# Kernel tuning notes

Measured on AMD Instinct MI355X. Metric: run time of the kernel, lower is better.

The kernel has to match this reference:

```python
import jax, jax.numpy as jnp
import numpy as np

B, T, D, H = 2, 2048, 1024, 16
HD = D // H  # head_dim = 64

def setup_inputs() -> dict:
    key = jax.random.key(0)
    ks = jax.random.split(key, 5)
    s = 0.02
    return {
        "x": jax.random.normal(ks[0], (B, T, D), dtype=jnp.float32),
        "w_qkv": jax.random.normal(ks[1], (3 * D, D), dtype=jnp.float32) * s,
        "b_qkv": jax.random.normal(ks[2], (3 * D,), dtype=jnp.float32) * s,
        "w_proj": jax.random.normal(ks[3], (D, D), dtype=jnp.float32) * s,
        "b_proj": jax.random.normal(ks[4], (D,), dtype=jnp.float32) * s,
    }

def reference(x, w_qkv, b_qkv, w_proj, b_proj):
    b, t, c = x.shape
    h, hd = H, HD
    scale = hd ** -0.5
    # qkv projection (torch Linear: x @ W^T + b)
    qkv = x @ w_qkv.T + b_qkv                      # [b, t, 3c]
    q, k, v = jnp.split(qkv, 3, axis=-1)
    # b t (h d) -> b h t d
    reshape = lambda z: z.reshape(b, t, h, hd).transpose(0, 2, 1, 3)
    q, k, v = reshape(q), reshape(k), reshape(v)
    scores = jnp.einsum("bhqd,bhkd->bhqk", q, k) * scale  # [b, h, t, t]
    causal = jnp.triu(jnp.ones((t, t), dtype=bool), k=1)   # True above diag
    scores = jnp.where(causal[None, None], -jnp.inf, scores)
    attn = jax.nn.softmax(scores, axis=-1)
    out = jnp.einsum("bhqk,bhkd->bhqd", attn, v)            # [b, h, t, d]
    out = out.transpose(0, 2, 1, 3).reshape(b, t, c)        # b h t d -> b t (h d)
    return out @ w_proj.T + b_proj
```

## Files before the change

kernel.cpp:

```cpp
#include <hip/hip_runtime.h>
#include <hip/hip_bf16.h>

#define Bq 2
#define Tq 2048
#define Dq 1024
#define Hq 16
#define HDq 64

typedef __attribute__((ext_vector_type(8))) short short8;
typedef __attribute__((ext_vector_type(4))) float f32x4;

__device__ __forceinline__ unsigned short f2bf(float f) {
  union { float f; unsigned int i; } v; v.f = f;
  unsigned int r = v.i + 0x7fffu + ((v.i >> 16) & 1u);
  return (unsigned short)(r >> 16);
}

__device__ __forceinline__ short8 cvt8(const float* __restrict__ g) {
  const float4* gp = (const float4*)g;
  float4 x0 = gp[0], x1 = gp[1];
  short8 v;
  v[0] = (short)f2bf(x0.x); v[1] = (short)f2bf(x0.y);
  v[2] = (short)f2bf(x0.z); v[3] = (short)f2bf(x0.w);
  v[4] = (short)f2bf(x1.x); v[5] = (short)f2bf(x1.y);
  v[6] = (short)f2bf(x1.z); v[7] = (short)f2bf(x1.w);
  return v;
}

__device__ __forceinline__ void async_cp16(const void* g, void* l) {
  __builtin_amdgcn_global_load_lds(
      (const __attribute__((address_space(1))) void*)g,
      (__attribute__((address_space(3))) void*)l, 16, 0, 0);
}

__device__ __forceinline__ void permswap(unsigned &a, unsigned &b) {
  asm("v_permlane32_swap_b32 %0, %1" : "+v"(a), "+v"(b));
  asm("v_permlane16_swap_b32 %0, %1" : "+v"(a), "+v"(b));
}

constexpr int NXC = (Bq * Tq * Dq) / 8;
constexpr int NW1C = (3 * Dq * Dq) / 8;
constexpr int NW2C = (Dq * Dq) / 8;

#define QSCL 0.18033688011112042f

__global__ __launch_bounds__(256)
void cvt_all(const float* __restrict__ x, const float* __restrict__ w1,
             const float* __restrict__ w2, unsigned short* __restrict__ xo,
             unsigned short* __restrict__ w1o, unsigned short* __restrict__ w2o)
{
  int i = blockIdx.x * 256 + threadIdx.x;
  const float* src; unsigned short* dst; int j;
  if (i < NXC)              { src = x;  dst = xo;  j = i; }
  else if (i < NXC + NW1C)  { src = w1; dst = w1o; j = i - NXC; }
  else                      { src = w2; dst = w2o; j = i - NXC - NW1C; }
  *(short8*)&dst[(size_t)j * 8] = cvt8(src + (size_t)j * 8);
}


__global__ __launch_bounds__(512, 2)
void gemm_qkv_8p(const unsigned short* __restrict__ Ab,
                 const unsigned short* __restrict__ Wb,
                 const float* __restrict__ bias, int K,
                 unsigned short* __restrict__ qo, unsigned short* __restrict__ ko,
                 unsigned short* __restrict__ vo)
{
  __shared__ unsigned short As[2][256 * 64];
  __shared__ unsigned short Bs[2][256 * 64];

  const int t = threadIdx.x;
  const int lane = t & 63, w = t >> 6;
  const int fr = lane & 15, qd = lane >> 4;
  const int wmi = w >> 2, wni = w & 3;
  const int m0 = blockIdx.y * 256, n0 = blockIdx.x * 256;
  const int arow_base = wmi * 128;
  const int brow_base = wni * 64;

  const int Gr0 = t >> 3;
  const int Gr1 = 64 + Gr0;
  const int Gc  = (t & 7) ^ (Gr0 & 7);

#define STAGE_HALF(kt1, hh, bufi) do {                                         \
    const unsigned short* _sb = ((hh) < 2) ? Ab + (size_t)m0 * K               \
                                           : Wb + (size_t)n0 * K;              \
    unsigned short* _lb = ((hh) < 2) ? &As[bufi][0] : &Bs[bufi][0];            \
    const int _h = (hh) & 1;                                                   \
    async_cp16(_sb + (size_t)(_h * 128 + Gr0) * K + (kt1) * 64 + Gc * 8,       \
               _lb + _h * 8192 + t * 8);                                       \
    async_cp16(_sb + (size_t)(_h * 128 + Gr1) * K + (kt1) * 64 + Gc * 8,       \
               _lb + _h * 8192 + 4096 + t * 8);                                \
  } while (0)

#define READ_AF(rg) do {                                                       \
    _Pragma("unroll")                                                          \
    for (int ibs = 0; ibs < 4; ibs++) {                                        \
      const int r = arow_base + (rg) * 64 + ibs * 16 + fr;                     \
      af[ibs][0] = *(const short8*)&As[c][r * 64 + ((qd ^ (r & 7)) * 8)];      \
      af[ibs][1] = *(const short8*)&As[c][r * 64 + (((4 + qd) ^ (r & 7)) * 8)];\
    } } while (0)

#define READ_BF(cg) do {                                                       \
    _Pragma("unroll")                                                          \
    for (int jbs = 0; jbs < 2; jbs++) {                                        \
      const int r = brow_base + (cg) * 32 + jbs * 16 + fr;                     \
      bf[jbs][0] = *(const short8*)&Bs[c][r * 64 + ((qd ^ (r & 7)) * 8)];      \
      bf[jbs][1] = *(const short8*)&Bs[c][r * 64 + (((4 + qd) ^ (r & 7)) * 8)];\
    } } while (0)

#define MM16(rg, cg) do {                                                      \
    __builtin_amdgcn_s_setprio(1);                                             \
    _Pragma("unroll")                                                          \
    for (int ibs = 0; ibs < 4; ibs++)                                          \
      _Pragma("unroll")                                                        \
      for (int jbs = 0; jbs < 2; jbs++) {                                      \
        acc[(rg)*4+ibs][(cg)*2+jbs] = __builtin_amdgcn_mfma_f32_16x16x32_bf16( \
            af[ibs][0], bf[jbs][0], acc[(rg)*4+ibs][(cg)*2+jbs], 0, 0, 0);     \
        acc[(rg)*4+ibs][(cg)*2+jbs] = __builtin_amdgcn_mfma_f32_16x16x32_bf16( \
            af[ibs][1], bf[jbs][1], acc[(rg)*4+ibs][(cg)*2+jbs], 0, 0, 0);     \
      }                                                                        \
    __builtin_amdgcn_s_setprio(0); } while (0)

#define BAR() do { asm volatile("" ::: "memory");                              \
    __builtin_amdgcn_s_barrier(); asm volatile("" ::: "memory"); } while (0)

  f32x4 acc[8][4] = {};
  short8 af[4][2], bf[2][2];

  STAGE_HALF(0, 0, 0); STAGE_HALF(0, 1, 0);
  STAGE_HALF(0, 2, 0); STAGE_HALF(0, 3, 0);

  const int KT = K >> 6;
  for (int kt = 0; kt < KT; kt++) {
    const int c = kt & 1;
    const bool pf = (kt + 1 < KT);
    if (pf) {
      STAGE_HALF(kt + 1, 0, c ^ 1);
      asm volatile("s_waitcnt vmcnt(2)" ::: "memory");
    } else {
      asm volatile("s_waitcnt vmcnt(0)" ::: "memory");
    }
    __builtin_amdgcn_s_barrier();
    READ_AF(0); READ_BF(0);
    BAR();
    MM16(0, 0);
    BAR();
    READ_BF(1);
    if (pf) STAGE_HALF(kt + 1, 1, c ^ 1);
    BAR();
    MM16(0, 1);
    BAR();
    READ_AF(1);
    if (pf) STAGE_HALF(kt + 1, 2, c ^ 1);
    BAR();
    MM16(1, 1);
    BAR();
    READ_BF(0);
    if (pf) STAGE_HALF(kt + 1, 3, c ^ 1);
    BAR();
    MM16(1, 0);
    BAR();
  }

  #pragma unroll
  for (int jb = 0; jb < 4; jb++) {
    int col = n0 + wni * 64 + jb * 16 + fr;
    float bv = bias[col];
    int which = col >> 10;
    int rem = col & 1023;
    int hh = rem >> 6, dd = rem & 63;
    #pragma unroll
    for (int ib = 0; ib < 8; ib++) {
      int row4 = m0 + wmi * 128 + ib * 16 + qd * 4;
      int bb = row4 >> 11, tt = row4 & (Tq - 1);
      if (which == 2) {
        unsigned lo = (unsigned)f2bf(acc[ib][jb][0] + bv)
                    | ((unsigned)f2bf(acc[ib][jb][1] + bv) << 16);
        unsigned hi = (unsigned)f2bf(acc[ib][jb][2] + bv)
                    | ((unsigned)f2bf(acc[ib][jb][3] + bv) << 16);
        uint2 pk; pk.x = lo; pk.y = hi;
        *(uint2*)&vo[((size_t)(bb * Hq + hh) * HDq + dd) * Tq + tt] = pk;
      } else {
        unsigned short* dst = (which == 0) ? qo : ko;
        float scl = (which == 0) ? QSCL : 1.0f;
        #pragma unroll
        for (int r = 0; r < 4; r++)
          dst[((size_t)(bb * Hq + hh) * Tq + tt + r) * HDq + dd] =
              f2bf((acc[ib][jb][r] + bv) * scl);
      }
    }
  }
#undef STAGE_HALF
#undef READ_AF
#undef READ_BF
#undef MM16
#undef BAR
}

template<int EPI, int BM_, int BN_>
__global__ __launch_bounds__(256)
void gemm_bt(const unsigned short* __restrict__ Ab, const unsigned short* __restrict__ Wb,
             const float* __restrict__ bias, float* __restrict__ outp,
             int K, int N,
             unsigned short* __restrict__ qo, unsigned short* __restrict__ ko,
             unsigned short* __restrict__ vo)
{
  constexpr int WM = BM_ / 2, WN = BN_ / 2;
  constexpr int NI = WM / 16;
  constexpr int NJ = WN / 16;
  constexpr int NAI = BM_ / 32;
  constexpr int NBI = BN_ / 32;
  __shared__ unsigned short As[2 * BM_ * 32];
  __shared__ unsigned short Bs[2 * BN_ * 32];

  const int t = threadIdx.x;
  const int lane = t & 63, w = t >> 6;
  const int m0 = blockIdx.y * BM_, n0 = blockIdx.x * BN_;
  const int fr = lane & 15, qd = lane >> 4;
  const int wm = (w >> 1) * WM, wn = (w & 1) * WN;

  f32x4 acc[NI][NJ] = {};

  for (int k0 = 0; k0 < K; k0 += 64) {
    __syncthreads();
    #pragma unroll
    for (int j = 0; j < NAI; j++) {
      int G = j * 256 + t;
      int panel = G / (BM_ * 4), rowg = (G / 4) % BM_, colg = G & 3;
      async_cp16(Ab + (size_t)(m0 + rowg) * K + k0 + panel * 32 + colg * 8, &As[G * 8]);
    }
    #pragma unroll
    for (int j = 0; j < NBI; j++) {
      int G = j * 256 + t;
      int panel = G / (BN_ * 4), rowg = (G / 4) % BN_, colg = G & 3;
      async_cp16(Wb + (size_t)(n0 + rowg) * K + k0 + panel * 32 + colg * 8, &Bs[G * 8]);
    }
    __syncthreads();
    #pragma unroll
    for (int kh = 0; kh < 2; kh++) {
      short8 af[NI], bf[NJ];
      #pragma unroll
      for (int ib = 0; ib < NI; ib++)
        af[ib] = *(const short8*)&As[kh * (BM_ * 32) + (wm + ib * 16 + fr) * 32 + qd * 8];
      #pragma unroll
      for (int jb = 0; jb < NJ; jb++)
        bf[jb] = *(const short8*)&Bs[kh * (BN_ * 32) + (wn + jb * 16 + fr) * 32 + qd * 8];
      #pragma unroll
      for (int ib = 0; ib < NI; ib++)
        #pragma unroll
        for (int jb = 0; jb < NJ; jb++)
          acc[ib][jb] = __builtin_amdgcn_mfma_f32_16x16x32_bf16(af[ib], bf[jb], acc[ib][jb], 0, 0, 0);
    }
  }

  #pragma unroll
  for (int jb = 0; jb < NJ; jb++) {
    int col = n0 + wn + jb * 16 + fr;
    float bv = bias[col];
    if (EPI == 0) {
      int which = col >> 10;
      int rem = col & 1023;
      int hh = rem >> 6, dd = rem & 63;
      #pragma unroll
      for (int ib = 0; ib < NI; ib++) {
        int row4 = m0 + wm + ib * 16 + qd * 4;
        int bb = row4 >> 11, tt = row4 & (Tq - 1);
        if (which == 2) {
          unsigned lo = (unsigned)f2bf(acc[ib][jb][0] + bv)
                      | ((unsigned)f2bf(acc[ib][jb][1] + bv) << 16);
          unsigned hi = (unsigned)f2bf(acc[ib][jb][2] + bv)
                      | ((unsigned)f2bf(acc[ib][jb][3] + bv) << 16);
          uint2 pk; pk.x = lo; pk.y = hi;
          *(uint2*)&vo[((size_t)(bb * Hq + hh) * HDq + dd) * Tq + tt] = pk;
        } else {
          unsigned short* dst = (which == 0) ? qo : ko;
          float scl = (which == 0) ? QSCL : 1.0f;
          #pragma unroll
          for (int r = 0; r < 4; r++)
            dst[((size_t)(bb * Hq + hh) * Tq + tt + r) * HDq + dd] =
                f2bf((acc[ib][jb][r] + bv) * scl);
        }
      }
    } else {
      #pragma unroll
      for (int ib = 0; ib < NI; ib++)
        #pragma unroll
        for (int r = 0; r < 4; r++) {
          int row = m0 + wm + ib * 16 + qd * 4 + r;
          outp[(size_t)row * N + col] = acc[ib][jb][r] + bv;
        }
    }
  }
}


template<bool DIAG>
__device__ __forceinline__ void strip_iter(
    const unsigned short* __restrict__ Ksb, const unsigned short* __restrict__ Vtsb,
    const short8 (&aq)[2], const short8 ones,
    int fr, int qd, int off0, int off1, int thr,
    f32x4 (&oacc)[4], f32x4& lacc)
{
  short8 bk[4][2];
  #pragma unroll
  for (int nb = 0; nb < 4; nb++) {
    bk[nb][0] = *(const short8*)&Ksb[(nb * 16 + fr) * 64 + off0];
    bk[nb][1] = *(const short8*)&Ksb[(nb * 16 + fr) * 64 + off1];
  }
  f32x4 s4[4] = {};
  __builtin_amdgcn_s_setprio(1);
  #pragma unroll
  for (int nb = 0; nb < 4; nb++)
    s4[nb] = __builtin_amdgcn_mfma_f32_16x16x32_bf16(bk[nb][0], aq[0], s4[nb], 0, 0, 0);
  #pragma unroll
  for (int nb = 0; nb < 4; nb++)
    s4[nb] = __builtin_amdgcn_mfma_f32_16x16x32_bf16(bk[nb][1], aq[1], s4[nb], 0, 0, 0);
  __builtin_amdgcn_s_setprio(0);

  unsigned x[4][2];
  #pragma unroll
  for (int nb = 0; nb < 4; nb++) {
    float p[4];
    #pragma unroll
    for (int reg = 0; reg < 4; reg++) {
      p[reg] = exp2f(s4[nb][reg]);
      if (DIAG && (nb * 16 + qd * 4 + reg) > thr) p[reg] = 0.f;
    }
    asm("v_cvt_pk_bf16_f32 %0, %1, %2" : "=v"(x[nb][0]) : "v"(p[0]), "v"(p[1]));
    asm("v_cvt_pk_bf16_f32 %0, %1, %2" : "=v"(x[nb][1]) : "v"(p[2]), "v"(p[3]));
  }
  permswap(x[0][0], x[1][0]);
  permswap(x[0][1], x[1][1]);
  permswap(x[2][0], x[3][0]);
  permswap(x[2][1], x[3][1]);

  short8 ap0, ap1;
  {
    union { unsigned u[4]; short8 s; } c0, c1;
    c0.u[0] = x[0][0]; c0.u[1] = x[0][1]; c0.u[2] = x[1][0]; c0.u[3] = x[1][1];
    c1.u[0] = x[2][0]; c1.u[1] = x[2][1]; c1.u[2] = x[3][0]; c1.u[3] = x[3][1];
    ap0 = c0.s; ap1 = c1.s;
  }

  short8 bv[4][2];
  #pragma unroll
  for (int db = 0; db < 4; db++) {
    bv[db][0] = *(const short8*)&Vtsb[(db * 16 + fr) * 64 + off0];
    bv[db][1] = *(const short8*)&Vtsb[(db * 16 + fr) * 64 + off1];
  }
  __builtin_amdgcn_s_setprio(1);
  lacc = __builtin_amdgcn_mfma_f32_16x16x32_bf16(ap0, ones, lacc, 0, 0, 0);
  lacc = __builtin_amdgcn_mfma_f32_16x16x32_bf16(ap1, ones, lacc, 0, 0, 0);
  #pragma unroll
  for (int db = 0; db < 4; db++) {
    oacc[db] = __builtin_amdgcn_mfma_f32_16x16x32_bf16(ap0, bv[db][0], oacc[db], 0, 0, 0);
    oacc[db] = __builtin_amdgcn_mfma_f32_16x16x32_bf16(ap1, bv[db][1], oacc[db], 0, 0, 0);
  }
  __builtin_amdgcn_s_setprio(0);
}

__global__ __launch_bounds__(256, 4)
void attn_fwd(const unsigned short* __restrict__ qb, const unsigned short* __restrict__ kb,
              const unsigned short* __restrict__ vtb, unsigned short* __restrict__ ab)
{
  __shared__ unsigned short Ks[2][64 * 64];
  __shared__ unsigned short Vts[2][64 * 64];

  const int t = threadIdx.x, w = t >> 6, lane = t & 63;
  const int fr = lane & 15, qd = lane >> 4;
  const int bh = blockIdx.x;
  const int s = 31 - (int)blockIdx.y;
  const int s0 = s * 64;
  const int thr = w * 16 + fr;

  short8 aq[2];
  const unsigned short* Qg = qb + ((size_t)bh * Tq + s0) * HDq;
  #pragma unroll
  for (int c = 0; c < 2; c++)
    aq[c] = *(const short8*)(Qg + (w * 16 + fr) * 64 + c * 32 + qd * 8);

  const unsigned short* Kbh = kb + (size_t)bh * Tq * HDq;
  const unsigned short* Vbh = vtb + (size_t)bh * HDq * Tq;

  const int off0 = ((qd ^ (fr & 7)) * 8);
  const int off1 = off0 ^ 32;

  const int G0 = 2 * w * 64 + lane, G1 = G0 + 64;
  const int r0 = G0 >> 3, g0 = (G0 & 7) ^ (r0 & 7);
  const int r1 = G1 >> 3, g1 = (G1 & 7) ^ (r1 & 7);

  short8 ones;
  #pragma unroll
  for (int j = 0; j < 8; j++) ones[j] = (short)0x3F80;

  f32x4 oacc[4] = {};
  f32x4 lacc = {};

  async_cp16(Kbh + (size_t)r0 * 64 + g0 * 8, &Ks[0][G0 * 8]);
  async_cp16(Vbh + (size_t)r0 * Tq + g0 * 8, &Vts[0][G0 * 8]);
  async_cp16(Kbh + (size_t)r1 * 64 + g1 * 8, &Ks[0][G1 * 8]);
  async_cp16(Vbh + (size_t)r1 * Tq + g1 * 8, &Vts[0][G1 * 8]);

  for (int kt = 0; kt < s; kt++) {
    const int cur = kt & 1, nxt = cur ^ 1;
    __syncthreads();
    const size_t kofs = (size_t)(kt + 1) * 64;
    async_cp16(Kbh + (kofs + r0) * 64 + g0 * 8, &Ks[nxt][G0 * 8]);
    async_cp16(Vbh + (size_t)r0 * Tq + kofs + g0 * 8, &Vts[nxt][G0 * 8]);
    async_cp16(Kbh + (kofs + r1) * 64 + g1 * 8, &Ks[nxt][G1 * 8]);
    async_cp16(Vbh + (size_t)r1 * Tq + kofs + g1 * 8, &Vts[nxt][G1 * 8]);
    strip_iter<false>(Ks[cur], Vts[cur], aq, ones, fr, qd, off0, off1, thr, oacc, lacc);
  }
  __syncthreads();
  strip_iter<true>(Ks[s & 1], Vts[s & 1], aq, ones, fr, qd, off0, off1, thr, oacc, lacc);

  #pragma unroll
  for (int reg = 0; reg < 4; reg++) {
    float linv = 1.0f / lacc[reg];
    size_t rowoff = ((size_t)(bh >> 4) * Tq + s0 + w * 16 + qd * 4 + reg) * Dq
                  + (bh & 15) * HDq;
    #pragma unroll
    for (int db = 0; db < 4; db++)
      ab[rowoff + db * 16 + fr] = f2bf(oacc[db][reg] * linv);
  }
}

extern "C" void kernel_launch(void* const* d_in, const int* in_sizes, int n_in,
                              void* d_out, int out_size, void* d_ws, size_t ws_size,
                              hipStream_t stream) {
  const float* x      = (const float*)d_in[0];
  const float* w_qkv  = (const float*)d_in[1];
  const float* b_qkv  = (const float*)d_in[2];
  const float* w_proj = (const float*)d_in[3];
  const float* b_proj = (const float*)d_in[4];
  float* out = (float*)d_out;

  unsigned short* ws = (unsigned short*)d_ws;
  const size_t NE = (size_t)Bq * Hq * Tq * HDq;
  unsigned short* qb  = ws;
  unsigned short* kb  = ws + NE;
  unsigned short* vtb = ws + 2 * NE;
  unsigned short* ab  = ws + 3 * NE;
  unsigned short* xb  = ws + 4 * NE;
  unsigned short* wqb = xb + (size_t)NXC * 8;
  unsigned short* wpb = wqb + (size_t)NW1C * 8;

  dim3 blk(256);
  cvt_all<<<dim3((NXC + NW1C + NW2C) >> 8), blk, 0, stream>>>(x, w_qkv, w_proj, xb, wqb, wpb);

  dim3 g1(3 * Dq / 256, Bq * Tq / 256);
  gemm_qkv_8p<<<g1, dim3(512), 0, stream>>>(xb, wqb, b_qkv, Dq, qb, kb, vtb);

  dim3 g2(Bq * Hq, Tq / 64);
  attn_fwd<<<g2, blk, 0, stream>>>(qb, kb, vtb, ab);

  dim3 g3(Dq / 128, Bq * Tq / 64);
  gemm_bt<1, 64, 128><<<g3, blk, 0, stream>>>(ab, wpb, b_proj, out,
                                              Dq, Dq, nullptr, nullptr, nullptr);
}
```

Baseline: 180.5 us.

## Retile QKV GEMM to 256x192 blocks with swizzled grid and bulk prefetch

After: 176.4 us. 2.2% less time.

```diff
diff --git a/kernel.cpp b/kernel.cpp
--- a/kernel.cpp
+++ b/kernel.cpp
@@ -66,106 +66,96 @@
                  unsigned short* __restrict__ vo)
 {
   __shared__ unsigned short As[2][256 * 64];
-  __shared__ unsigned short Bs[2][256 * 64];
+  __shared__ unsigned short Bs[2][192 * 64];
 
   const int t = threadIdx.x;
   const int lane = t & 63, w = t >> 6;
   const int fr = lane & 15, qd = lane >> 4;
   const int wmi = w >> 2, wni = w & 3;
-  const int m0 = blockIdx.y * 256, n0 = blockIdx.x * 256;
+  const int lin = (int)blockIdx.y * 16 + (int)blockIdx.x;
+  const int swz = (lin & 7) * 32 + (lin >> 3);
+  const int bxs = swz & 15, bys = swz >> 4;
+  const int m0 = bys * 256, n0 = bxs * 192;
   const int arow_base = wmi * 128;
-  const int brow_base = wni * 64;
-
-  const int Gr0 = t >> 3;
-  const int Gr1 = 64 + Gr0;
-  const int Gc  = (t & 7) ^ (Gr0 & 7);
-
-#define STAGE_HALF(kt1, hh, bufi) do {                                         \
-    const unsigned short* _sb = ((hh) < 2) ? Ab + (size_t)m0 * K               \
-                                           : Wb + (size_t)n0 * K;              \
-    unsigned short* _lb = ((hh) < 2) ? &As[bufi][0] : &Bs[bufi][0];            \
-    const int _h = (hh) & 1;                                                   \
-    async_cp16(_sb + (size_t)(_h * 128 + Gr0) * K + (kt1) * 64 + Gc * 8,       \
-               _lb + _h * 8192 + t * 8);                                       \
-    async_cp16(_sb + (size_t)(_h * 128 + Gr1) * K + (kt1) * 64 + Gc * 8,       \
-               _lb + _h * 8192 + 4096 + t * 8);                                \
+  const int brow_base = wni * 48;
+
+#define STAGE_A(kt1, bufi) do {                                                \
+    _Pragma("unroll")                                                          \
+    for (int j = 0; j < 4; j++) {                                              \
+      int G = j * 512 + t;                                                     \
+      int row = G >> 3, cg = (G & 7) ^ (row & 7);                              \
+      async_cp16(Ab + (size_t)(m0 + row) * K + (kt1) * 64 + cg * 8,            \
+                 &As[bufi][G * 8]);                                            \
+    } } while (0)
+
+#define STAGE_B(kt1, bufi) do {                                                \
+    _Pragma("unroll")                                                          \
+    for (int j = 0; j < 3; j++) {                                              \
+      int G = j * 512 + t;                                                     \
+      int row = G >> 3, cg = (G & 7) ^ (row & 7);                              \
+      async_cp16(Wb + (size_t)(n0 + row) * K + (kt1) * 64 + cg * 8,            \
+                 &Bs[bufi][G * 8]);                                            \
+    } } while (0)
+
+#define READ_AF_ALL() do {                                                     \
+    _Pragma("unroll")                                                          \
+    for (int ib = 0; ib < 8; ib++) {                                           \
+      const int r = arow_base + ib * 16 + fr;                                  \
+      af[ib][0] = *(const short8*)&As[c][r * 64 + ((qd ^ (r & 7)) * 8)];       \
+      af[ib][1] = *(const short8*)&As[c][r * 64 + (((4 + qd) ^ (r & 7)) * 8)]; \
+    } } while (0)
+
+#define READ_BF(cg) do {                                                       \
+    const int r = brow_base + (cg) * 16 + fr;                                  \
+    bf[0] = *(const short8*)&Bs[c][r * 64 + ((qd ^ (r & 7)) * 8)];             \
+    bf[1] = *(const short8*)&Bs[c][r * 64 + (((4 + qd) ^ (r & 7)) * 8)];       \
   } while (0)
 
-#define READ_AF(rg) do {                                                       \
-    _Pragma("unroll")                                                          \
-    for (int ibs = 0; ibs < 4; ibs++) {                                        \
-      const int r = arow_base + (rg) * 64 + ibs * 16 + fr;                     \
-      af[ibs][0] = *(const short8*)&As[c][r * 64 + ((qd ^ (r & 7)) * 8)];      \
-      af[ibs][1] = *(const short8*)&As[c][r * 64 + (((4 + qd) ^ (r & 7)) * 8)];\
-    } } while (0)
-
-#define READ_BF(cg) do {                                                       \
-    _Pragma("unroll")                                                          \
-    for (int jbs = 0; jbs < 2; jbs++) {                                        \
-      const int r = brow_base + (cg) * 32 + jbs * 16 + fr;                     \
-      bf[jbs][0] = *(const short8*)&Bs[c][r * 64 + ((qd ^ (r & 7)) * 8)];      \
-      bf[jbs][1] = *(const short8*)&Bs[c][r * 64 + (((4 + qd) ^ (r & 7)) * 8)];\
-    } } while (0)
-
-#define MM16(rg, cg) do {                                                      \
+#define MM16(cg) do {                                                          \
     __builtin_amdgcn_s_setprio(1);                                             \
     _Pragma("unroll")                                                          \
-    for (int ibs = 0; ibs < 4; ibs++)                                          \
-      _Pragma("unroll")                                                        \
-      for (int jbs = 0; jbs < 2; jbs++) {                                      \
-        acc[(rg)*4+ibs][(cg)*2+jbs] = __builtin_amdgcn_mfma_f32_16x16x32_bf16( \
-            af[ibs][0], bf[jbs][0], acc[(rg)*4+ibs][(cg)*2+jbs], 0, 0, 0);     \
-        acc[(rg)*4+ibs][(cg)*2+jbs] = __builtin_amdgcn_mfma_f32_16x16x32_bf16( \
-            af[ibs][1], bf[jbs][1], acc[(rg)*4+ibs][(cg)*2+jbs], 0, 0, 0);     \
-      }                                                                        \
+    for (int ib = 0; ib < 8; ib++) {                                           \
+      acc[ib][cg] = __builtin_amdgcn_mfma_f32_16x16x32_bf16(                   \
+          af[ib][0], bf[0], acc[ib][cg], 0, 0, 0);                             \
+      acc[ib][cg] = __builtin_amdgcn_mfma_f32_16x16x32_bf16(                   \
+          af[ib][1], bf[1], acc[ib][cg], 0, 0, 0);                             \
+    }                                                                          \
     __builtin_amdgcn_s_setprio(0); } while (0)
 
 #define BAR() do { asm volatile("" ::: "memory");                              \
     __builtin_amdgcn_s_barrier(); asm volatile("" ::: "memory"); } while (0)
 
-  f32x4 acc[8][4] = {};
-  short8 af[4][2], bf[2][2];
-
-  STAGE_HALF(0, 0, 0); STAGE_HALF(0, 1, 0);
-  STAGE_HALF(0, 2, 0); STAGE_HALF(0, 3, 0);
+  f32x4 acc[8][3] = {};
+  short8 af[8][2], bf[2];
+
+  STAGE_A(0, 0); STAGE_B(0, 0);
 
   const int KT = K >> 6;
   for (int kt = 0; kt < KT; kt++) {
     const int c = kt & 1;
-    const bool pf = (kt + 1 < KT);
-    if (pf) {
-      STAGE_HALF(kt + 1, 0, c ^ 1);
-      asm volatile("s_waitcnt vmcnt(2)" ::: "memory");
+    if (kt + 1 < KT) {
+      STAGE_A(kt + 1, c ^ 1);
+      STAGE_B(kt + 1, c ^ 1);
+      asm volatile("s_waitcnt vmcnt(7)" ::: "memory");
     } else {
       asm volatile("s_waitcnt vmcnt(0)" ::: "memory");
     }
     __builtin_amdgcn_s_barrier();
-    READ_AF(0); READ_BF(0);
-    BAR();
-    MM16(0, 0);
-    BAR();
+    READ_AF_ALL();
+    READ_BF(0);
+    BAR(); MM16(0); BAR();
     READ_BF(1);
-    if (pf) STAGE_HALF(kt + 1, 1, c ^ 1);
-    BAR();
-    MM16(0, 1);
-    BAR();
-    READ_AF(1);
-    if (pf) STAGE_HALF(kt + 1, 2, c ^ 1);
-    BAR();
-    MM16(1, 1);
-    BAR();
-    READ_BF(0);
-    if (pf) STAGE_HALF(kt + 1, 3, c ^ 1);
-    BAR();
-    MM16(1, 0);
-    BAR();
-  }
-
-  #pragma unroll
-  for (int jb = 0; jb < 4; jb++) {
-    int col = n0 + wni * 64 + jb * 16 + fr;
+    BAR(); MM16(1); BAR();
+    READ_BF(2);
+    BAR(); MM16(2); BAR();
+  }
+
+  #pragma unroll
+  for (int jb = 0; jb < 3; jb++) {
+    int colbase = n0 + wni * 48 + jb * 16;
+    int col = colbase + fr;
     float bv = bias[col];
-    int which = col >> 10;
+    int which = colbase >> 10;
     int rem = col & 1023;
     int hh = rem >> 6, dd = rem & 63;
     #pragma unroll
@@ -189,8 +179,9 @@
       }
     }
   }
-#undef STAGE_HALF
-#undef READ_AF
+#undef STAGE_A
+#undef STAGE_B
+#undef READ_AF_ALL
 #undef READ_BF
 #undef MM16
 #undef BAR
@@ -447,7 +438,7 @@
   dim3 blk(256);
   cvt_all<<<dim3((NXC + NW1C + NW2C) >> 8), blk, 0, stream>>>(x, w_qkv, w_proj, xb, wqb, wpb);
 
-  dim3 g1(3 * Dq / 256, Bq * Tq / 256);
+  dim3 g1(16, 16);
   gemm_qkv_8p<<<g1, dim3(512), 0, stream>>>(xb, wqb, b_qkv, Dq, qb, kb, vtb);
 
   dim3 g2(Bq * Hq, Tq / 64);
```
